# Kernel tuning notes

Hardware: AMD Instinct MI355X
Metric: run time of the kernel (lower is better)

Reference implementation:

```python
import jax, jax.numpy as jnp
import numpy as np

B, N, C = 1, 768, 384
H, P = 12, 4
DP = 128  # dim_pair
HP3 = H * P * 3  # 144


def linear(x, W, b):
    # torch nn.Linear: y = x @ W.T + b, W shape (out, in)
    return jnp.einsum('...i,oi->...o', x, W) + b


def setup_inputs() -> dict:
    key = jax.random.key(0)
    ks = jax.random.split(key, 24)
    w = lambda k, *s: jax.random.normal(k, s, jnp.float32) * 0.02
    inp = {
        'single': jax.random.normal(ks[0], (B, N, C), jnp.float32),
        'pair': jax.random.normal(ks[1], (B, N, N, DP), jnp.float32),
        'rot': jax.random.normal(ks[2], (B, N, 3, 3), jnp.float32),
        'trans': jax.random.normal(ks[3], (B, N, 3), jnp.float32),
        'Wq': w(ks[4], C, C), 'bq': jnp.zeros((C,), jnp.float32),
        'Wk': w(ks[5], C, C), 'bk': jnp.zeros((C,), jnp.float32),
        'Wv': w(ks[6], C, C), 'bv': jnp.zeros((C,), jnp.float32),
        'Wpb': w(ks[7], H, DP), 'bpb': jnp.zeros((H,), jnp.float32),
        'Wqp': w(ks[8], HP3, C), 'bqp': jnp.zeros((HP3,), jnp.float32),
        'Wkp': w(ks[9], HP3, C), 'bkp': jnp.zeros((HP3,), jnp.float32),
        'Wvp': w(ks[10], HP3, C), 'bvp': jnp.zeros((HP3,), jnp.float32),
        'Wo': w(ks[11], C, C), 'bo': jnp.zeros((C,), jnp.float32),
        'Wpo': w(ks[12], C, HP3), 'bpo': jnp.zeros((C,), jnp.float32),
        'ln_w': jnp.ones((C,), jnp.float32), 'ln_b': jnp.zeros((C,), jnp.float32),
    }
    return inp


def reference(single, pair, rot, trans, Wq, bq, Wk, bk, Wv, bv, Wpb, bpb,
              Wqp, bqp, Wkp, bkp, Wvp, bvp, Wo, bo, Wpo, bpo, ln_w, ln_b):
    Ch = C // H
    scale = Ch ** -0.5
    q = linear(single, Wq, bq).reshape(B, N, H, Ch)
    k = linear(single, Wk, bk).reshape(B, N, H, Ch)
    v = linear(single, Wv, bv).reshape(B, N, H, Ch)
    pair_bias = jnp.transpose(linear(pair, Wpb, bpb), (0, 3, 1, 2))  # (B,H,N,N)

    q_pts = linear(single, Wqp, bqp).reshape(B, N, H, P, 3)
    k_pts = linear(single, Wkp, bkp).reshape(B, N, H, P, 3)
    v_pts = linear(single, Wvp, bvp).reshape(B, N, H, P, 3)
    t = trans[:, :, None, None, :]  # (B,N,1,1,3)
    # rotate local points into global frame: p @ R + t
    q_g = jnp.einsum('bnhpd,bnde->bnhpe', q_pts, rot) + t
    k_g = jnp.einsum('bnhpd,bnde->bnhpe', k_pts, rot) + t
    v_g = jnp.einsum('bnhpd,bnde->bnhpe', v_pts, rot) + t

    q2 = jnp.sum(q_g ** 2, axis=(3, 4))  # (B,N,H)
    k2 = jnp.sum(k_g ** 2, axis=(3, 4))
    qk = jnp.einsum('bnhpd,bmhpd->bhnm', q_g, k_g)
    q2h = jnp.transpose(q2, (0, 2, 1))  # (B,H,N)
    k2h = jnp.transpose(k2, (0, 2, 1))
    point_logits = -0.5 * (q2h[..., :, None] + k2h[..., None, :] - 2.0 * qk) * scale
    scalar_logits = jnp.einsum('bnhc,bmhc->bhnm', q, k) * scale
    attn = jax.nn.softmax(scalar_logits + pair_bias + point_logits, axis=-1)

    weighted_scalar = jnp.einsum('bhnm,bmhc->bnhc', attn, v).reshape(B, N, C)
    weighted_points = jnp.einsum('bhnm,bmhpd->bnhpd', attn, v_g).reshape(B, N, HP3)
    point_proj = linear(weighted_points, Wpo, bpo)
    out = linear(weighted_scalar + point_proj, Wo, bo)

    x = single + out
    mu = jnp.mean(x, axis=-1, keepdims=True)
    var = jnp.mean((x - mu) ** 2, axis=-1, keepdims=True)
    return (x - mu) / jnp.sqrt(var + 1e-5) * ln_w + ln_b
```

## Files before the change

### kernel.cpp

```cpp
#include <hip/hip_runtime.h>
#include <math.h>

#define NRES 768
#define CDIM 384
#define HEADS 12
#define SCALE 0.17677669529663687f

typedef _Float16 f16;
typedef _Float16 __attribute__((ext_vector_type(8))) f16x8;
typedef float __attribute__((ext_vector_type(4))) f32x4;

__device__ __forceinline__ f16x8 ldcvt8(const float* __restrict__ p) {
  float4 a = *(const float4*)p;
  float4 b = *(const float4*)(p + 4);
  f16x8 r = {(f16)a.x, (f16)a.y, (f16)a.z, (f16)a.w,
             (f16)b.x, (f16)b.y, (f16)b.z, (f16)b.w};
  return r;
}

__device__ __forceinline__ void mfma_step(f16 (*As)[64], f16 (*Bs)[64],
                                          int w, int lg, int lr, f32x4* acc) {
#pragma unroll
  for (int ks = 0; ks < 2; ++ks) {
    f16x8 af = *(const f16x8*)&As[w * 16 + lr][((ks * 4 + lg) ^ (lr & 7)) * 8];
#pragma unroll
    for (int c = 0; c < 4; ++c) {
      f16x8 bf = *(const f16x8*)&Bs[c * 16 + lr][((ks * 4 + lg) ^ (lr & 7)) * 8];
      acc[c] = __builtin_amdgcn_mfma_f32_16x16x32_f16(af, bf, acc[c], 0, 0, 0);
    }
  }
}

__global__ __launch_bounds__(256) void mega_gemm(
    const float* __restrict__ single,
    const float* __restrict__ Wq, const float* __restrict__ Wk, const float* __restrict__ Wv,
    const float* __restrict__ Wqp, const float* __restrict__ Wkp, const float* __restrict__ Wvp,
    const float* __restrict__ bq, const float* __restrict__ bk, const float* __restrict__ bv,
    const float* __restrict__ bqp, const float* __restrict__ bkp, const float* __restrict__ bvp,
    const float* __restrict__ Wpo, const float* __restrict__ bpo, const float* __restrict__ Wo,
    f16* __restrict__ Wcomb, f16* __restrict__ S16) {
  __shared__ f16 As[64][64];
  __shared__ f16 Bs[64][64];
  const int bx = blockIdx.x, by = blockIdx.y;
  const int t = threadIdx.x;
  const int w = t >> 6, l = t & 63;
  const int lg = l >> 4, lr = l & 15;
  const f16 z0 = (f16)0.f;
  f32x4 acc[4] = {{0.f,0.f,0.f,0.f},{0.f,0.f,0.f,0.f},{0.f,0.f,0.f,0.f},{0.f,0.f,0.f,0.f}};

  if (bx < 25) {
    const int bm = by * 64, bn = bx * 64;
    for (int k0 = 0; k0 < 384; k0 += 64) {
      __syncthreads();
#pragma unroll
      for (int cc = 0; cc < 2; ++cc) {
        int c = t + cc * 256;
        int row = c >> 3, k8 = c & 7;
        int sw = (k8 ^ (row & 7)) * 8;
        *(f16x8*)&As[row][sw] = ldcvt8(single + (size_t)(bm + row) * 384 + k0 + k8 * 8);
        int o = bn + row;
        const float* bsrc;
        if (o < 384)       bsrc = Wq  + (size_t)o * 384;
        else if (o < 768)  bsrc = Wk  + (size_t)(o - 384) * 384;
        else if (o < 1152) bsrc = Wv  + (size_t)(o - 768) * 384;
        else if (o < 1296) bsrc = Wqp + (size_t)(o - 1152) * 384;
        else if (o < 1440) bsrc = Wkp + (size_t)(o - 1296) * 384;
        else if (o < 1584) bsrc = Wvp + (size_t)(o - 1440) * 384;
        else               bsrc = nullptr;
        f16x8 vb8 = {z0, z0, z0, z0, z0, z0, z0, z0};
        if (bsrc) vb8 = ldcvt8(bsrc + k0 + k8 * 8);
        *(f16x8*)&Bs[row][sw] = vb8;
      }
      __syncthreads();
      mfma_step(As, Bs, w, lg, lr, acc);
    }
#pragma unroll
    for (int c = 0; c < 4; ++c) {
      int col = bn + c * 16 + lr;
      if (col >= 1584) continue;
      float bb;
      if (col < 384)       bb = bq[col];
      else if (col < 768)  bb = bk[col - 384];
      else if (col < 1152) bb = bv[col - 768];
      else if (col < 1296) bb = bqp[col - 1152];
      else if (col < 1440) bb = bkp[col - 1296];
      else                 bb = bvp[col - 1440];
#pragma unroll
      for (int r = 0; r < 4; ++r) {
        int row = bm + w * 16 + lg * 4 + r;
        S16[(size_t)row * 1584 + col] = (f16)(acc[c][r] + bb);
      }
    }
  } else if (by < 6) {
    const int bm = by * 64, bn = (bx - 25) * 64;
    for (int k0 = 0; k0 < 384; k0 += 64) {
      __syncthreads();
#pragma unroll
      for (int cc = 0; cc < 2; ++cc) {
        int c = t + cc * 256;
        int row = c >> 3, k8 = c & 7;
        int sw = (k8 ^ (row & 7)) * 8;
        *(f16x8*)&As[row][sw] = ldcvt8(Wo + (size_t)(bm + row) * 384 + k0 + k8 * 8);
        int pr = bn + row;
        f16x8 vb8 = {z0, z0, z0, z0, z0, z0, z0, z0};
        if (pr < 144) {
#pragma unroll
          for (int j = 0; j < 8; ++j) vb8[j] = (f16)Wpo[(size_t)(k0 + k8 * 8 + j) * 144 + pr];
        } else if (pr == 144) {
#pragma unroll
          for (int j = 0; j < 8; ++j) vb8[j] = (f16)bpo[k0 + k8 * 8 + j];
        }
        *(f16x8*)&Bs[row][sw] = vb8;
      }
      __syncthreads();
      mfma_step(As, Bs, w, lg, lr, acc);
    }
#pragma unroll
    for (int c = 0; c < 4; ++c) {
      int col = bn + c * 16 + lr;
      if (col >= 192) continue;
#pragma unroll
      for (int r = 0; r < 4; ++r)
        Wcomb[(size_t)(bm + w * 16 + lg * 4 + r) * 192 + col] = (f16)acc[c][r];
    }
  }
}

__global__ __launch_bounds__(256) void final_gemm(
    const f16* __restrict__ attn_cat, const float* __restrict__ Wo,
    const f16* __restrict__ Wcomb, const float* __restrict__ bo,
    const float* __restrict__ single, float* __restrict__ xb) {
  __shared__ f16 As[64][64];
  __shared__ f16 Bs[64][64];
  const int t = threadIdx.x;
  const int w = t >> 6, l = t & 63;
  const int lg = l >> 4, lr = l & 15;
  const int bm = blockIdx.y * 64, bn = blockIdx.x * 64;
  f32x4 acc[4] = {{0.f,0.f,0.f,0.f},{0.f,0.f,0.f,0.f},{0.f,0.f,0.f,0.f},{0.f,0.f,0.f,0.f}};
  for (int k0 = 0; k0 < 576; k0 += 64) {
    __syncthreads();
#pragma unroll
    for (int cc = 0; cc < 2; ++cc) {
      int c = t + cc * 256;
      int row = c >> 3, k8 = c & 7;
      int sw = (k8 ^ (row & 7)) * 8;
      *(f16x8*)&As[row][sw] = *(const f16x8*)(attn_cat + (size_t)(bm + row) * 576 + k0 + k8 * 8);
      f16x8 vb8;
      if (k0 < 384) vb8 = ldcvt8(Wo + (size_t)(bn + row) * 384 + k0 + k8 * 8);
      else          vb8 = *(const f16x8*)(Wcomb + (size_t)(bn + row) * 192 + (k0 - 384) + k8 * 8);
      *(f16x8*)&Bs[row][sw] = vb8;
    }
    __syncthreads();
    mfma_step(As, Bs, w, lg, lr, acc);
  }
#pragma unroll
  for (int c = 0; c < 4; ++c) {
    int col = bn + c * 16 + lr;
    float bb = bo[col];
#pragma unroll
    for (int r = 0; r < 4; ++r) {
      int row = bm + w * 16 + lg * 4 + r;
      xb[(size_t)row * 384 + col] = acc[c][r] + bb + single[(size_t)row * 384 + col];
    }
  }
}

__global__ __launch_bounds__(256) void rot_feats3(
    const f16* __restrict__ S16, const float* __restrict__ rot, const float* __restrict__ trans,
    f16* __restrict__ qf, f16* __restrict__ kf, f16* __restrict__ vfT) {
  const int n = blockIdx.x * 256 + threadIdx.x;
  const int h = blockIdx.y;
  const f16* Sr = S16 + (size_t)n * 1584;
  float R[9], T[3];
#pragma unroll
  for (int i = 0; i < 9; ++i) R[i] = rot[n * 9 + i];
#pragma unroll
  for (int i = 0; i < 3; ++i) T[i] = trans[n * 3 + i];
  f16 qh[64], kh[64];
  f16x8 qv4[4], kv4[4], vv4[4];
#pragma unroll
  for (int j = 0; j < 4; ++j) {
    qv4[j] = *(const f16x8*)(Sr + h * 32 + j * 8);
    kv4[j] = *(const f16x8*)(Sr + 384 + h * 32 + j * 8);
    vv4[j] = *(const f16x8*)(Sr + 768 + h * 32 + j * 8);
  }
#pragma unroll
  for (int c = 0; c < 32; ++c) {
    qh[c] = (f16)(SCALE * (float)qv4[c >> 3][c & 7]);
    vfT[((size_t)(h * 48 + c)) * NRES + n] = vv4[c >> 3][c & 7];
  }
#pragma unroll
  for (int j = 0; j < 4; ++j) *(f16x8*)&kh[j * 8] = kv4[j];
  float qp[12], kp[12], vp[12];
#pragma unroll
  for (int e = 0; e < 12; ++e) {
    qp[e] = (float)Sr[1152 + h * 12 + e];
    kp[e] = (float)Sr[1296 + h * 12 + e];
    vp[e] = (float)Sr[1440 + h * 12 + e];
  }
  float q2 = 0.f, k2 = 0.f;
#pragma unroll
  for (int p = 0; p < 4; ++p) {
#pragma unroll
    for (int e = 0; e < 3; ++e) {
      float qg = qp[p*3+0] * R[e] + qp[p*3+1] * R[3+e] + qp[p*3+2] * R[6+e] + T[e];
      float kg = kp[p*3+0] * R[e] + kp[p*3+1] * R[3+e] + kp[p*3+2] * R[6+e] + T[e];
      float vg = vp[p*3+0] * R[e] + vp[p*3+1] * R[3+e] + vp[p*3+2] * R[6+e] + T[e];
      qh[32 + p*3 + e] = (f16)(SCALE * qg); q2 += qg * qg;
      kh[32 + p*3 + e] = (f16)kg;           k2 += kg * kg;
      vfT[((size_t)(h * 48 + 32 + p*3 + e)) * NRES + n] = (f16)vg;
    }
  }
  qh[44] = (f16)(-0.5f * SCALE * q2); qh[45] = (f16)1.f;
  kh[44] = (f16)1.f;                  kh[45] = (f16)(-0.5f * SCALE * k2);
#pragma unroll
  for (int c = 46; c < 64; ++c) { qh[c] = (f16)0.f; kh[c] = (f16)0.f; }
#pragma unroll
  for (int c = 44; c < 48; ++c) vfT[((size_t)(h * 48 + c)) * NRES + n] = (f16)0.f;
  f16* qo = qf + ((size_t)(h * NRES + n)) * 64;
  f16* ko = kf + ((size_t)(h * NRES + n)) * 64;
#pragma unroll
  for (int j = 0; j < 8; ++j) {
    *(f16x8*)&qo[j * 8] = *(const f16x8*)&qh[j * 8];
    *(f16x8*)&ko[j * 8] = *(const f16x8*)&kh[j * 8];
  }
}

__global__ __launch_bounds__(512) void fused_attn(
    const float* __restrict__ pair, const float* __restrict__ Wpb, const float* __restrict__ bpb,
    const f16* __restrict__ qf, const f16* __restrict__ kf, const f16* __restrict__ vfT,
    f16* __restrict__ partNh, float* __restrict__ partD) {
  __shared__ f16 bias_l[12 * 1160];
  __shared__ f16 p_l[8][1160];
  const int t = threadIdx.x;
  const int w = t >> 6, l = t & 63;
  const int lg = l >> 4, lr = l & 15;
  const int mblk = blockIdx.x;
  const int q0 = blockIdx.y * 16;
  const int m0 = mblk * 64;

  f16x8 bfr[4];
#pragma unroll
  for (int ks = 0; ks < 4; ++ks)
#pragma unroll
    for (int j = 0; j < 8; ++j)
      bfr[ks][j] = (f16)((lr < HEADS) ? Wpb[lr * 128 + ks * 32 + lg * 8 + j] : 0.f);
  const float bh = (lr < HEADS) ? bpb[lr] : 0.f;

#pragma unroll
  for (int g8 = 0; g8 < 8; ++g8) {
    const int g = w * 8 + g8;
    const int rowf = g * 16 + lr;
    const int nf = rowf >> 6, mf = rowf & 63;
    const float* ap = pair + (((size_t)(q0 + nf)) * NRES + (m0 + mf)) * 128 + lg * 8;
    f32x4 acc = {0.f, 0.f, 0.f, 0.f};
#pragma unroll
    for (int ks = 0; ks < 4; ++ks) {
      float4 a0 = *(const float4*)(ap + ks * 32);
      float4 a1 = *(const float4*)(ap + ks * 32 + 4);
      f16x8 af = {(f16)a0.x, (f16)a0.y, (f16)a0.z, (f16)a0.w,
                  (f16)a1.x, (f16)a1.y, (f16)a1.z, (f16)a1.w};
      acc = __builtin_amdgcn_mfma_f32_16x16x32_f16(af, bfr[ks], acc, 0, 0, 0);
    }
    if (lr < HEADS) {
#pragma unroll
      for (int r = 0; r < 4; ++r) {
        int rowo = g * 16 + lg * 4 + r;
        bias_l[lr * 1160 + (rowo >> 6) * 72 + (rowo & 63)] = (f16)(acc[r] + bh);
      }
    }
  }
  __syncthreads();

  for (int h = w; h < 12; h += 8) {
    const f16* qrow = qf + ((size_t)(h * NRES + q0 + lr)) * 64;
    f16x8 qa0 = *(const f16x8*)(qrow + lg * 8);
    f16x8 qa1 = *(const f16x8*)(qrow + 32 + lg * 8);
    float den[4] = {0.f, 0.f, 0.f, 0.f};
#pragma unroll
    for (int mc = 0; mc < 4; ++mc) {
      const f16* krow = kf + ((size_t)(h * NRES + m0 + mc * 16 + lr)) * 64;
      f16x8 kb0 = *(const f16x8*)(krow + lg * 8);
      f16x8 kb1 = *(const f16x8*)(krow + 32 + lg * 8);
      f32x4 s = {0.f, 0.f, 0.f, 0.f};
      s = __builtin_amdgcn_mfma_f32_16x16x32_f16(qa0, kb0, s, 0, 0, 0);
      s = __builtin_amdgcn_mfma_f32_16x16x32_f16(qa1, kb1, s, 0, 0, 0);
#pragma unroll
      for (int r = 0; r < 4; ++r) {
        float b = (float)bias_l[h * 1160 + (lg * 4 + r) * 72 + mc * 16 + lr];
        float e = __expf(s[r] + b);
        den[r] += e;
        p_l[w][(lg * 4 + r) * 72 + mc * 16 + lr] = (f16)e;
      }
    }
#pragma unroll
    for (int r = 0; r < 4; ++r) {
      float d = den[r];
      d += __shfl_xor(d, 1); d += __shfl_xor(d, 2);
      d += __shfl_xor(d, 4); d += __shfl_xor(d, 8);
      if (lr == 0)
        partD[((size_t)mblk * NRES + q0 + lg * 4 + r) * 12 + h] = d;
    }
#pragma unroll
    for (int c3 = 0; c3 < 3; ++c3) {
      f32x4 a = {0.f, 0.f, 0.f, 0.f};
#pragma unroll
      for (int ks = 0; ks < 2; ++ks) {
        f16x8 pa = *(const f16x8*)&p_l[w][lr * 72 + ks * 32 + lg * 8];
        f16x8 vb = *(const f16x8*)(vfT + ((size_t)(h * 48 + c3 * 16 + lr)) * NRES + m0 + ks * 32 + lg * 8);
        a = __builtin_amdgcn_mfma_f32_16x16x32_f16(pa, vb, a, 0, 0, 0);
      }
#pragma unroll
      for (int r = 0; r < 4; ++r)
        partNh[((size_t)mblk * NRES + q0 + lg * 4 + r) * 576 + h * 48 + c3 * 16 + lr] = (f16)a[r];
    }
  }
}

__global__ __launch_bounds__(576) void attn_reduce(
    const f16* __restrict__ partNh, const float* __restrict__ partD,
    f16* __restrict__ attn_cat) {
  const int n = blockIdx.x;
  const int hc = threadIdx.x;
  const int h = hc / 48, c = hc - h * 48;
  float num = 0.f, den = 0.f;
#pragma unroll
  for (int mc = 0; mc < 12; ++mc) {
    num += (float)partNh[((size_t)mc * NRES + n) * 576 + hc];
    den += partD[((size_t)mc * NRES + n) * 12 + h];
  }
  float val = num / den;
  if (c < 32)      attn_cat[(size_t)n * 576 + h * 32 + c] = (f16)val;
  else if (c < 44) attn_cat[(size_t)n * 576 + 384 + h * 12 + (c - 32)] = (f16)val;
  if (hc < 48)     attn_cat[(size_t)n * 576 + 528 + hc] = (f16)(hc == 0 ? 1.f : 0.f);
}

__global__ __launch_bounds__(64) void ln_kernel(
    const float* __restrict__ x, const float* __restrict__ w, const float* __restrict__ b,
    float* __restrict__ out) {
  int n = blockIdx.x;
  int l = threadIdx.x;
  const float* xr = x + (size_t)n * CDIM;
  float v[6];
  float s = 0.f;
#pragma unroll
  for (int i = 0; i < 6; ++i) { v[i] = xr[l + 64 * i]; s += v[i]; }
#pragma unroll
  for (int o = 32; o; o >>= 1) s += __shfl_xor(s, o);
  float mu = s * (1.f / 384.f);
  float vs = 0.f;
#pragma unroll
  for (int i = 0; i < 6; ++i) { float d = v[i] - mu; vs += d * d; }
#pragma unroll
  for (int o = 32; o; o >>= 1) vs += __shfl_xor(vs, o);
  float rstd = rsqrtf(vs * (1.f / 384.f) + 1e-5f);
  float* orow = out + (size_t)n * CDIM;
#pragma unroll
  for (int i = 0; i < 6; ++i) {
    int c = l + 64 * i;
    orow[c] = (v[i] - mu) * rstd * w[c] + b[c];
  }
}

extern "C" void kernel_launch(void* const* d_in, const int* in_sizes, int n_in,
                              void* d_out, int out_size, void* d_ws, size_t ws_size,
                              hipStream_t stream) {
  const float* single = (const float*)d_in[0];
  const float* pair   = (const float*)d_in[1];
  const float* rot    = (const float*)d_in[2];
  const float* trans  = (const float*)d_in[3];
  const float* Wq  = (const float*)d_in[4];
  const float* bq  = (const float*)d_in[5];
  const float* Wk  = (const float*)d_in[6];
  const float* bk  = (const float*)d_in[7];
  const float* Wv  = (const float*)d_in[8];
  const float* bv  = (const float*)d_in[9];
  const float* Wpb = (const float*)d_in[10];
  const float* bpb = (const float*)d_in[11];
  const float* Wqp = (const float*)d_in[12];
  const float* bqp = (const float*)d_in[13];
  const float* Wkp = (const float*)d_in[14];
  const float* bkp = (const float*)d_in[15];
  const float* Wvp = (const float*)d_in[16];
  const float* bvp = (const float*)d_in[17];
  const float* Wo  = (const float*)d_in[18];
  const float* bo  = (const float*)d_in[19];
  const float* Wpo = (const float*)d_in[20];
  const float* bpo = (const float*)d_in[21];
  const float* lnw = (const float*)d_in[22];
  const float* lnb = (const float*)d_in[23];

  float* ws = (float*)d_ws;
  f16* S16      = (f16*)ws; ws += 768 * 1584 / 2;
  f16* Wcomb    = (f16*)ws; ws += 384 * 192 / 2;
  f16* qf       = (f16*)ws; ws += 12 * 768 * 64 / 2;
  f16* kf       = (f16*)ws; ws += 12 * 768 * 64 / 2;
  f16* vfT      = (f16*)ws; ws += 12 * 48 * 768 / 2;
  f16* partNh   = (f16*)ws; ws += 12 * 768 * 576 / 2;
  float* partD  = ws;       ws += 12 * 768 * 12;
  f16* attn_cat = (f16*)ws; ws += 768 * 576 / 2;
  float* xb     = ws;       ws += 768 * 384;

  mega_gemm<<<dim3(28, 12), 256, 0, stream>>>(single,
                                              Wq, Wk, Wv, Wqp, Wkp, Wvp,
                                              bq, bk, bv, bqp, bkp, bvp,
                                              Wpo, bpo, Wo, Wcomb, S16);
  rot_feats3<<<dim3(3, 12), 256, 0, stream>>>(S16, rot, trans, qf, kf, vfT);
  fused_attn<<<dim3(12, 48), 512, 0, stream>>>(pair, Wpb, bpb, qf, kf, vfT, partNh, partD);
  attn_reduce<<<768, 576, 0, stream>>>(partNh, partD, attn_cat);
  final_gemm<<<dim3(6, 12), 256, 0, stream>>>(attn_cat, Wo, Wcomb, bo, single, xb);
  ln_kernel<<<768, 64, 0, stream>>>(xb, lnw, lnb, (float*)d_out);
}
```

Baseline: 135.4 us.

## Fuse LayerNorm into final GEMM via atomic row stats and last-block finalize

```diff
diff --git a/kernel.cpp b/kernel.cpp
--- a/kernel.cpp
+++ b/kernel.cpp
@@ -126,12 +126,17 @@
   }
 }
 
-__global__ __launch_bounds__(256) void final_gemm(
+__global__ __launch_bounds__(256) void final_gemm_ln(
     const f16* __restrict__ attn_cat, const float* __restrict__ Wo,
     const f16* __restrict__ Wcomb, const float* __restrict__ bo,
-    const float* __restrict__ single, float* __restrict__ xb) {
+    const float* __restrict__ single, float* __restrict__ xb,
+    float* __restrict__ rowsum, float* __restrict__ rowsumsq,
+    unsigned* __restrict__ counter,
+    const float* __restrict__ lnw, const float* __restrict__ lnb,
+    float* __restrict__ out) {
   __shared__ f16 As[64][64];
   __shared__ f16 Bs[64][64];
+  __shared__ unsigned done_s;
   const int t = threadIdx.x;
   const int w = t >> 6, l = t & 63;
   const int lg = l >> 4, lr = l & 15;
@@ -160,15 +165,44 @@
 #pragma unroll
     for (int r = 0; r < 4; ++r) {
       int row = bm + w * 16 + lg * 4 + r;
-      xb[(size_t)row * 384 + col] = acc[c][r] + bb + single[(size_t)row * 384 + col];
-    }
-  }
-}
-
-__global__ __launch_bounds__(256) void rot_feats3(
+      float v = acc[c][r] + bb + single[(size_t)row * 384 + col];
+      acc[c][r] = v;
+      xb[(size_t)row * 384 + col] = v;
+    }
+  }
+#pragma unroll
+  for (int r = 0; r < 4; ++r) {
+    float s = acc[0][r] + acc[1][r] + acc[2][r] + acc[3][r];
+    float sq = acc[0][r]*acc[0][r] + acc[1][r]*acc[1][r] + acc[2][r]*acc[2][r] + acc[3][r]*acc[3][r];
+    s  += __shfl_xor(s, 1);  s  += __shfl_xor(s, 2);  s  += __shfl_xor(s, 4);  s  += __shfl_xor(s, 8);
+    sq += __shfl_xor(sq, 1); sq += __shfl_xor(sq, 2); sq += __shfl_xor(sq, 4); sq += __shfl_xor(sq, 8);
+    if (lr == 0) {
+      int row = bm + w * 16 + lg * 4 + r;
+      atomicAdd(&rowsum[row], s);
+      atomicAdd(&rowsumsq[row], sq);
+    }
+  }
+  __threadfence();
+  if (t == 0) done_s = atomicAdd(&counter[blockIdx.y], 1u);
+  __syncthreads();
+  if (done_s == 5) {
+    __threadfence();
+    for (int i = t; i < 64 * 384; i += 256) {
+      int row = bm + (i / 384), col = i % 384;
+      float rs = rowsum[row], rq = rowsumsq[row];
+      float mu = rs * (1.f / 384.f);
+      float var = rq * (1.f / 384.f) - mu * mu;
+      float rstd = rsqrtf(var + 1e-5f);
+      float v = xb[(size_t)row * 384 + col];
+      out[(size_t)row * 384 + col] = (v - mu) * rstd * lnw[col] + lnb[col];
+    }
+  }
+}
+
+__global__ __launch_bounds__(64) void rot_feats3(
     const f16* __restrict__ S16, const float* __restrict__ rot, const float* __restrict__ trans,
     f16* __restrict__ qf, f16* __restrict__ kf, f16* __restrict__ vfT) {
-  const int n = blockIdx.x * 256 + threadIdx.x;
+  const int n = blockIdx.x * 64 + threadIdx.x;
   const int h = blockIdx.y;
   const f16* Sr = S16 + (size_t)n * 1584;
   float R[9], T[3];
@@ -319,10 +353,13 @@
 
 __global__ __launch_bounds__(576) void attn_reduce(
     const f16* __restrict__ partNh, const float* __restrict__ partD,
-    f16* __restrict__ attn_cat) {
+    f16* __restrict__ attn_cat,
+    float* __restrict__ rowsum, float* __restrict__ rowsumsq, unsigned* __restrict__ counter) {
   const int n = blockIdx.x;
   const int hc = threadIdx.x;
   const int h = hc / 48, c = hc - h * 48;
+  if (hc == 0) { rowsum[n] = 0.f; rowsumsq[n] = 0.f; }
+  if (n == 0 && hc < 12) counter[hc] = 0u;
   float num = 0.f, den = 0.f;
 #pragma unroll
   for (int mc = 0; mc < 12; ++mc) {
@@ -333,33 +370,6 @@
   if (c < 32)      attn_cat[(size_t)n * 576 + h * 32 + c] = (f16)val;
   else if (c < 44) attn_cat[(size_t)n * 576 + 384 + h * 12 + (c - 32)] = (f16)val;
   if (hc < 48)     attn_cat[(size_t)n * 576 + 528 + hc] = (f16)(hc == 0 ? 1.f : 0.f);
-}
-
-__global__ __launch_bounds__(64) void ln_kernel(
-    const float* __restrict__ x, const float* __restrict__ w, const float* __restrict__ b,
-    float* __restrict__ out) {
-  int n = blockIdx.x;
-  int l = threadIdx.x;
-  const float* xr = x + (size_t)n * CDIM;
-  float v[6];
-  float s = 0.f;
-#pragma unroll
-  for (int i = 0; i < 6; ++i) { v[i] = xr[l + 64 * i]; s += v[i]; }
-#pragma unroll
-  for (int o = 32; o; o >>= 1) s += __shfl_xor(s, o);
-  float mu = s * (1.f / 384.f);
-  float vs = 0.f;
-#pragma unroll
-  for (int i = 0; i < 6; ++i) { float d = v[i] - mu; vs += d * d; }
-#pragma unroll
-  for (int o = 32; o; o >>= 1) vs += __shfl_xor(vs, o);
-  float rstd = rsqrtf(vs * (1.f / 384.f) + 1e-5f);
-  float* orow = out + (size_t)n * CDIM;
-#pragma unroll
-  for (int i = 0; i < 6; ++i) {
-    int c = l + 64 * i;
-    orow[c] = (v[i] - mu) * rstd * w[c] + b[c];
-  }
 }
 
 extern "C" void kernel_launch(void* const* d_in, const int* in_sizes, int n_in,
@@ -400,14 +410,18 @@
   float* partD  = ws;       ws += 12 * 768 * 12;
   f16* attn_cat = (f16*)ws; ws += 768 * 576 / 2;
   float* xb     = ws;       ws += 768 * 384;
+  float* rowsum = ws;       ws += 768;
+  float* rowsumsq = ws;     ws += 768;
+  unsigned* counter = (unsigned*)ws; ws += 16;
 
   mega_gemm<<<dim3(28, 12), 256, 0, stream>>>(single,
                                               Wq, Wk, Wv, Wqp, Wkp, Wvp,
                                               bq, bk, bv, bqp, bkp, bvp,
                                               Wpo, bpo, Wo, Wcomb, S16);
-  rot_feats3<<<dim3(3, 12), 256, 0, stream>>>(S16, rot, trans, qf, kf, vfT);
+  rot_feats3<<<dim3(12, 12), 64, 0, stream>>>(S16, rot, trans, qf, kf, vfT);
   fused_attn<<<dim3(12, 48), 512, 0, stream>>>(pair, Wpb, bpb, qf, kf, vfT, partNh, partD);
-  attn_reduce<<<768, 576, 0, stream>>>(partNh, partD, attn_cat);
-  final_gemm<<<dim3(6, 12), 256, 0, stream>>>(attn_cat, Wo, Wcomb, bo, single, xb);
-  ln_kernel<<<768, 64, 0, stream>>>(xb, lnw, lnb, (float*)d_out);
-}
+  attn_reduce<<<768, 576, 0, stream>>>(partNh, partD, attn_cat, rowsum, rowsumsq, counter);
+  final_gemm_ln<<<dim3(6, 12), 256, 0, stream>>>(attn_cat, Wo, Wcomb, bo, single, xb,
+                                                 rowsum, rowsumsq, counter, lnw, lnb,
+                                                 (float*)d_out);
+}
```

After: 173.4 us. 28.0% more time.
